# Performance work log

Hardware: AMD Instinct MI355X
Metric: run time of the kernel (lower is better)

## Reference

```python
import jax, jax.numpy as jnp
import numpy as np

D_MODEL = 256
N_HEAD = 8
D_FF = 1024
B = 8
N_PER = 4096
NQ = B * N_PER
L = 16
NEG_INF = -1e9
EPS = 1e-5


def layer_norm(x, g, b):
    mu = jnp.mean(x, axis=-1, keepdims=True)
    var = jnp.mean(jnp.square(x - mu), axis=-1, keepdims=True)
    return (x - mu) * jax.lax.rsqrt(var + EPS) * g + b


def setup_inputs() -> dict:
    key = jax.random.key(0)
    ks = jax.random.split(key, 20)
    s = 1.0 / np.sqrt(D_MODEL)
    sf = 1.0 / np.sqrt(D_FF)
    inp = {
        "src": jax.random.normal(ks[0], (NQ, D_MODEL), jnp.float32),
        "pos": jax.random.normal(ks[1], (NQ, D_MODEL), jnp.float32),
        # per-batch-relative neighbor indices in [-1, N_PER); -1 == invalid/padded
        "index_pair": jax.random.randint(ks[2], (NQ, L), 0, N_PER + 1, jnp.int32) - 1,
        "query_batch_cnt": jnp.full((B,), N_PER, jnp.int32),
        "key_batch_cnt": jnp.full((B,), N_PER, jnp.int32),
        "index_pair_batch": (jnp.arange(NQ, dtype=jnp.int32) // N_PER).astype(jnp.int32),
        "Wq": jax.random.normal(ks[3], (D_MODEL, D_MODEL), jnp.float32) * s,
        "bq": jnp.zeros((D_MODEL,), jnp.float32),
        "Wk": jax.random.normal(ks[4], (D_MODEL, D_MODEL), jnp.float32) * s,
        "bk": jnp.zeros((D_MODEL,), jnp.float32),
        "Wv": jax.random.normal(ks[5], (D_MODEL, D_MODEL), jnp.float32) * s,
        "bv": jnp.zeros((D_MODEL,), jnp.float32),
        "Wo": jax.random.normal(ks[6], (D_MODEL, D_MODEL), jnp.float32) * s,
        "bo": jnp.zeros((D_MODEL,), jnp.float32),
        "W1": jax.random.normal(ks[7], (D_MODEL, D_FF), jnp.float32) * s,
        "b1": jnp.zeros((D_FF,), jnp.float32),
        "W2": jax.random.normal(ks[8], (D_FF, D_MODEL), jnp.float32) * sf,
        "b2": jnp.zeros((D_MODEL,), jnp.float32),
        "g1": jnp.ones((D_MODEL,), jnp.float32),
        "be1": jnp.zeros((D_MODEL,), jnp.float32),
        "g2": jnp.ones((D_MODEL,), jnp.float32),
        "be2": jnp.zeros((D_MODEL,), jnp.float32),
    }
    return inp


def local_attn(q, k, v, index_pair, key_batch_cnt, index_pair_batch,
               Wq, bq, Wk, bk, Wv, bv, Wo, bo):
    H, hd = N_HEAD, D_MODEL // N_HEAD
    scale = 1.0 / np.sqrt(hd)
    qh = (q @ Wq + bq).reshape(NQ, H, hd) * scale        # [Nq,H,hd]
    kh = (k @ Wk + bk).reshape(NQ, H, hd)                # [Nk,H,hd] (Nk==Nq)
    vh = (v @ Wv + bv).reshape(NQ, H, hd)
    # start offset of each batch's keys in the stacked key tensor
    offs = jnp.cumsum(key_batch_cnt) - key_batch_cnt      # [B]
    valid = index_pair >= 0                               # [Nq,L]
    gidx = jnp.where(valid, index_pair + offs[index_pair_batch][:, None], 0)
    k_g = kh[gidx]                                        # [Nq,L,H,hd]
    v_g = vh[gidx]                                        # [Nq,L,H,hd]
    logits = jnp.einsum('nhd,nlhd->nhl', qh, k_g)         # [Nq,H,L]
    logits = jnp.where(valid[:, None, :], logits, NEG_INF)
    attn = jax.nn.softmax(logits, axis=-1)
    out = jnp.einsum('nhl,nlhd->nhd', attn, v_g).reshape(NQ, D_MODEL)
    return out @ Wo + bo


def reference(src, pos, index_pair, query_batch_cnt, key_batch_cnt, index_pair_batch,
              Wq, bq, Wk, bk, Wv, bv, Wo, bo, W1, b1, W2, b2, g1, be1, g2, be2):
    # forward_post (normalize_before=False), dropout==0 (eval)
    qk = src + pos
    src2 = local_attn(qk, qk, src, index_pair, key_batch_cnt, index_pair_batch,
                      Wq, bq, Wk, bk, Wv, bv, Wo, bo)
    x = layer_norm(src + src2, g1, be1)
    ff = jax.nn.relu(x @ W1 + b1) @ W2 + b2
    return layer_norm(x + ff, g2, be2)
```

## Files before the change

kernel.cpp:

```cpp
#include <hip/hip_runtime.h>
#include <hip/hip_bf16.h>
#include <cstdint>
#include <cstddef>

#define NQ_ 32768
#define DM_ 256
#define DFF_ 1024
#define LNB_ 16
#define NB_ 8

typedef __attribute__((ext_vector_type(4))) float f32x4;
typedef __attribute__((ext_vector_type(8))) short s16x8;

__device__ __forceinline__ float bf2f(ushort u) {
    union { unsigned int i; float f; } c; c.i = ((unsigned int)u) << 16; return c.f;
}
__device__ __forceinline__ ushort f2bf(float f) {
    union { float f; unsigned int i; } c; c.f = f;
    unsigned int x = c.i;
    return (ushort)((x + 0x7fffu + ((x >> 16) & 1u)) >> 16);
}


__global__ __launch_bounds__(256) void prep_qk(const float* __restrict__ src, const float* __restrict__ pos,
                                               ushort* __restrict__ qkb, ushort* __restrict__ srcb) {
    int i = (blockIdx.x * 256 + threadIdx.x) * 4;
    float4 s = *(const float4*)(src + i);
    float4 p = *(const float4*)(pos + i);
    ushort4 a, b;
    a.x = f2bf(s.x + p.x); a.y = f2bf(s.y + p.y); a.z = f2bf(s.z + p.z); a.w = f2bf(s.w + p.w);
    b.x = f2bf(s.x);       b.y = f2bf(s.y);       b.z = f2bf(s.z);       b.w = f2bf(s.w);
    *(ushort4*)(qkb + i) = a;
    *(ushort4*)(srcb + i) = b;
}

__global__ __launch_bounds__(256) void prep_weights(const float* __restrict__ Wq, const float* __restrict__ Wk,
                                                    const float* __restrict__ Wv, const float* __restrict__ Wo,
                                                    const float* __restrict__ W1, const float* __restrict__ W2,
                                                    const int* __restrict__ kbc,
                                                    const float* __restrict__ bq, const float* __restrict__ bk,
                                                    ushort* __restrict__ WqT, ushort* __restrict__ WkT,
                                                    ushort* __restrict__ WvT, ushort* __restrict__ WoT,
                                                    ushort* __restrict__ W1T, ushort* __restrict__ W2T,
                                                    int* __restrict__ offs, float* __restrict__ bias2) {
    const int b = blockIdx.x;
    const int t = threadIdx.x;
    if (b == 3072) {
        if (t == 0) { int a = 0; for (int i = 0; i < NB_; ++i) { offs[i] = a; a += kbc[i]; } }
        bias2[t] = bq[t];
        bias2[256 + t] = bk[t];
        return;
    }
    const float* W; ushort* Wt; int base, ks, ns;
    if (b < 1024) {
        const int sec = b >> 8;
        W  = sec == 0 ? Wq  : sec == 1 ? Wk  : sec == 2 ? Wv  : Wo;
        Wt = sec == 0 ? WqT : sec == 1 ? WkT : sec == 2 ? WvT : WoT;
        base = (b & 255) * 256; ks = 8; ns = 8;
    } else if (b < 2048) {
        W = W1; Wt = W1T; base = (b - 1024) * 256; ks = 8; ns = 10;
    } else {
        W = W2; Wt = W2T; base = (b - 2048) * 256; ks = 10; ns = 8;
    }
    const int i = base + t;
    const int n = i >> ks, k = i & ((1 << ks) - 1);
    Wt[i] = f2bf(W[(k << ns) + n]);
}


__device__ __forceinline__ void gld_lds16(const ushort* g, ushort* l) {
    __builtin_amdgcn_global_load_lds((const __attribute__((address_space(1))) void*)g,
                                     (__attribute__((address_space(3))) void*)l, 16, 0, 0);
}

template <bool RELU>
__global__ __launch_bounds__(256) void gemm_kernel(const ushort* __restrict__ A, const ushort* __restrict__ Bt,
                                                   const float* __restrict__ bias, ushort* __restrict__ C,
                                                   int M, int N, int K, float alpha) {
    __shared__ __align__(16) ushort As[2 * 128 * 32];
    __shared__ __align__(16) ushort Bs[2 * 128 * 32];
    const int tid = threadIdx.x;
    const int lane = tid & 63;
    const int wave = tid >> 6;
    const int wr = wave >> 1, wc = wave & 1;

    const int b = (int)(blockIdx.y * gridDim.x + blockIdx.x);
    const int idx = b >> 3;
    const int xt = (b & 7) * 32 + (idx & 31);
    const int yt = idx >> 5;
    const long m0 = (long)xt * 128;
    const long n0 = (long)yt * 128;

    f32x4 acc[4][4] = {};

    const int c0 = tid, c1 = tid + 256;
    const int ar0 = c0 >> 2, ac0 = c0 & 3;
    const int ar1 = c1 >> 2, ac1 = c1 & 3;
    const int as0 = (ac0 ^ ((ar0 >> 1) & 3)) * 8;
    const int as1 = (ac1 ^ ((ar1 >> 1) & 3)) * 8;
    const int la = lane & 15;
    const int sx = ((lane >> 4) ^ ((la >> 1) & 3)) * 8;

    const ushort* Ar0 = A + (m0 + ar0) * K + as0;
    const ushort* Ar1 = A + (m0 + ar1) * K + as1;
    const ushort* Br0 = Bt + (n0 + ar0) * K + as0;
    const ushort* Br1 = Bt + (n0 + ar1) * K + as1;

    const int nt = K >> 5;
    int boff = 0;
    gld_lds16(Ar0, As + c0 * 8);
    gld_lds16(Ar1, As + c1 * 8);
    gld_lds16(Br0, Bs + c0 * 8);
    gld_lds16(Br1, Bs + c1 * 8);

    for (int t = 0; t < nt; ++t) {
        if (t + 1 < nt) {
            const int kt = (t + 1) << 5;
            const int nb = boff ^ 4096;
            gld_lds16(Ar0 + kt, As + nb + c0 * 8);
            gld_lds16(Ar1 + kt, As + nb + c1 * 8);
            gld_lds16(Br0 + kt, Bs + nb + c0 * 8);
            gld_lds16(Br1 + kt, Bs + nb + c1 * 8);
            asm volatile("s_waitcnt vmcnt(4)" ::: "memory");
        } else {
            asm volatile("s_waitcnt vmcnt(0)" ::: "memory");
        }
        __builtin_amdgcn_s_barrier();
        s16x8 af[4], bfr[4];
#pragma unroll
        for (int m = 0; m < 4; ++m)
            af[m] = *(const s16x8*)(As + boff + (wr * 64 + m * 16 + la) * 32 + sx);
#pragma unroll
        for (int n = 0; n < 4; ++n)
            bfr[n] = *(const s16x8*)(Bs + boff + (wc * 64 + n * 16 + la) * 32 + sx);
        asm volatile("s_waitcnt lgkmcnt(0)" ::: "memory");
        __builtin_amdgcn_s_barrier();
#pragma unroll
        for (int m = 0; m < 4; ++m)
#pragma unroll
            for (int n = 0; n < 4; ++n)
                acc[m][n] = __builtin_amdgcn_mfma_f32_16x16x32_bf16(af[m], bfr[n], acc[m][n], 0, 0, 0);
        boff ^= 4096;
    }

#pragma unroll
    for (int n = 0; n < 4; ++n) {
        const long col = n0 + wc * 64 + n * 16 + la;
        const float bv = bias[col];
#pragma unroll
        for (int m = 0; m < 4; ++m) {
#pragma unroll
            for (int j = 0; j < 4; ++j) {
                const long row = m0 + wr * 64 + m * 16 + (lane >> 4) * 4 + j;
                float r = (acc[m][n][j] + bv) * alpha;
                if (RELU) r = fmaxf(r, 0.f);
                C[row * N + col] = f2bf(r);
            }
        }
    }
}


template <bool F32OUT>
__global__ __launch_bounds__(256) void gemm_ln_kernel(const ushort* __restrict__ A, const ushort* __restrict__ Bt,
                                                      const float* __restrict__ bias,
                                                      const ushort* __restrict__ resid,
                                                      const float* __restrict__ g, const float* __restrict__ be,
                                                      void* __restrict__ outv, int K) {
    __shared__ __align__(16) ushort As[2 * 64 * 32];
    __shared__ __align__(16) ushort Bs[2 * 256 * 32];
    __shared__ float red_s[4][64];
    __shared__ float red_q[4][64];
    const int tid = threadIdx.x;
    const int lane = tid & 63;
    const int wave = tid >> 6;
    const long m0 = (long)blockIdx.x * 64;

    const int ca = tid;
    const ushort* Arow = A + (m0 + (ca >> 2)) * K + ((ca & 3) ^ ((ca >> 3) & 3)) * 8;
    const ushort* Brow[4];
#pragma unroll
    for (int i = 0; i < 4; ++i) {
        const int cb = tid + 256 * i;
        Brow[i] = Bt + (long)(cb >> 2) * K + ((cb & 3) ^ ((cb >> 3) & 3)) * 8;
    }
    const int la = lane & 15;
    const int sx = ((lane >> 4) ^ ((la >> 1) & 3)) * 8;

    f32x4 acc[4][4] = {};
    const int nt = K >> 5;
    int buf = 0;
    gld_lds16(Arow, As + ca * 8);
#pragma unroll
    for (int i = 0; i < 4; ++i)
        gld_lds16(Brow[i], Bs + (tid + 256 * i) * 8);

    for (int t = 0; t < nt; ++t) {
        const int bA = buf * 2048, bB = buf * 8192;
        if (t + 1 < nt) {
            const int kt = (t + 1) << 5;
            const int nA = (buf ^ 1) * 2048, nB = (buf ^ 1) * 8192;
            gld_lds16(Arow + kt, As + nA + ca * 8);
#pragma unroll
            for (int i = 0; i < 4; ++i)
                gld_lds16(Brow[i] + kt, Bs + nB + (tid + 256 * i) * 8);
            asm volatile("s_waitcnt vmcnt(5)" ::: "memory");
        } else {
            asm volatile("s_waitcnt vmcnt(0)" ::: "memory");
        }
        __builtin_amdgcn_s_barrier();
        s16x8 af[4], bfr[4];
#pragma unroll
        for (int m = 0; m < 4; ++m)
            af[m] = *(const s16x8*)(As + bA + (m * 16 + la) * 32 + sx);
#pragma unroll
        for (int n = 0; n < 4; ++n)
            bfr[n] = *(const s16x8*)(Bs + bB + (wave * 64 + n * 16 + la) * 32 + sx);
        asm volatile("s_waitcnt lgkmcnt(0)" ::: "memory");
        __builtin_amdgcn_s_barrier();
#pragma unroll
        for (int m = 0; m < 4; ++m)
#pragma unroll
            for (int n = 0; n < 4; ++n)
                acc[m][n] = __builtin_amdgcn_mfma_f32_16x16x32_bf16(af[m], bfr[n], acc[m][n], 0, 0, 0);
        buf ^= 1;
    }

    const int rg4 = (lane >> 4) * 4;
    float bv[4];
#pragma unroll
    for (int n = 0; n < 4; ++n) bv[n] = bias[wave * 64 + n * 16 + la];

#pragma unroll
    for (int m = 0; m < 4; ++m) {
#pragma unroll
        for (int j = 0; j < 4; ++j) {
            const int lr = m * 16 + rg4 + j;
            float s = 0.f, q = 0.f;
#pragma unroll
            for (int n = 0; n < 4; ++n) {
                const int col = wave * 64 + n * 16 + la;
                float v = acc[m][n][j] + bv[n] + bf2f(resid[(m0 + lr) * DM_ + col]);
                acc[m][n][j] = v;
                s += v; q += v * v;
            }
#pragma unroll
            for (int mk = 1; mk < 16; mk <<= 1) { s += __shfl_xor(s, mk); q += __shfl_xor(q, mk); }
            if (la == 0) { red_s[wave][lr] = s; red_q[wave][lr] = q; }
        }
    }
    __syncthreads();

    float gv[4], bev[4];
#pragma unroll
    for (int n = 0; n < 4; ++n) {
        const int col = wave * 64 + n * 16 + la;
        gv[n] = g[col]; bev[n] = be[col];
    }
#pragma unroll
    for (int m = 0; m < 4; ++m) {
#pragma unroll
        for (int j = 0; j < 4; ++j) {
            const int lr = m * 16 + rg4 + j;
            const float s = red_s[0][lr] + red_s[1][lr] + red_s[2][lr] + red_s[3][lr];
            const float q = red_q[0][lr] + red_q[1][lr] + red_q[2][lr] + red_q[3][lr];
            const float mu = s * (1.f / 256.f);
            const float rsig = rsqrtf(q * (1.f / 256.f) - mu * mu + 1e-5f);
#pragma unroll
            for (int n = 0; n < 4; ++n) {
                const int col = wave * 64 + n * 16 + la;
                const float r = (acc[m][n][j] - mu) * rsig * gv[n] + bev[n];
                if (F32OUT) ((float*)outv)[(m0 + lr) * DM_ + col] = r;
                else        ((ushort*)outv)[(m0 + lr) * DM_ + col] = f2bf(r);
            }
        }
    }
}


__global__ __launch_bounds__(256, 4) void attn_kernel(const ushort* __restrict__ QKb,
                                                      const ushort* __restrict__ Vb, const int* __restrict__ ipair,
                                                      const int* __restrict__ ipb, const int* __restrict__ offs,
                                                      ushort* __restrict__ Ob) {
    const int blk = (blockIdx.x & 7) * (NQ_ / 8 / 8) + (blockIdx.x >> 3);
    const int lane = threadIdx.x & 63;
    const int n = blk * 8 + (threadIdx.x >> 6) * 2 + (lane >> 5);
    const size_t hoff = (size_t)(lane & 31) * 8;

    float q[8];
    {
        s16x8 v = *(const s16x8*)(QKb + (size_t)n * 512 + hoff);
#pragma unroll
        for (int e = 0; e < 8; ++e) q[e] = bf2f((ushort)v[e]);
    }
    const int off = offs[ipb[n]];
    int gi[LNB_];
    float lg[LNB_];
#pragma unroll
    for (int j = 0; j < LNB_; ++j) {
        const int ip = ipair[n * LNB_ + j];
        const int g = ip >= 0 ? ip + off : 0;
        gi[j] = g;
        s16x8 v = *(const s16x8*)(QKb + (size_t)g * 512 + 256 + hoff);
        float p = 0.f;
#pragma unroll
        for (int e = 0; e < 8; ++e)
            p = fmaf(q[e], bf2f((ushort)v[e]), p);
        p += __shfl_xor(p, 1);
        p += __shfl_xor(p, 2);
        lg[j] = ip >= 0 ? p * 0.17677669529663688f : -1e9f;
    }
    float mx = lg[0];
#pragma unroll
    for (int j = 1; j < LNB_; ++j) mx = fmaxf(mx, lg[j]);
    float sum = 0.f, pw[LNB_];
#pragma unroll
    for (int j = 0; j < LNB_; ++j) { pw[j] = __expf(lg[j] - mx); sum += pw[j]; }
    const float inv = 1.f / sum;

    float acc[8] = {};
#pragma unroll
    for (int j = 0; j < LNB_; ++j) {
        s16x8 v = *(const s16x8*)(Vb + (size_t)gi[j] * DM_ + hoff);
        const float w = pw[j] * inv;
#pragma unroll
        for (int e = 0; e < 8; ++e)
            acc[e] = fmaf(w, bf2f((ushort)v[e]), acc[e]);
    }
    s16x8 o;
#pragma unroll
    for (int e = 0; e < 8; ++e) o[e] = (short)f2bf(acc[e]);
    *(s16x8*)(Ob + (size_t)n * DM_ + hoff) = o;
}


extern "C" void kernel_launch(void* const* d_in, const int* in_sizes, int n_in,
                              void* d_out, int out_size, void* d_ws, size_t ws_size,
                              hipStream_t stream) {
    const float* src = (const float*)d_in[0];
    const float* pos = (const float*)d_in[1];
    const int* ipair = (const int*)d_in[2];
    const int* kbc   = (const int*)d_in[4];
    const int* ipb   = (const int*)d_in[5];
    const float* Wq = (const float*)d_in[6];  const float* bq = (const float*)d_in[7];
    const float* Wk = (const float*)d_in[8];  const float* bk = (const float*)d_in[9];
    const float* Wv = (const float*)d_in[10]; const float* bv = (const float*)d_in[11];
    const float* Wo = (const float*)d_in[12]; const float* bo = (const float*)d_in[13];
    const float* W1 = (const float*)d_in[14]; const float* b1 = (const float*)d_in[15];
    const float* W2 = (const float*)d_in[16]; const float* b2 = (const float*)d_in[17];
    const float* g1 = (const float*)d_in[18]; const float* be1 = (const float*)d_in[19];
    const float* g2 = (const float*)d_in[20]; const float* be2 = (const float*)d_in[21];

    char* ws = (char*)d_ws;
    const size_t SB = (size_t)NQ_ * DM_ * 2;
    ushort* qkb  = (ushort*)(ws);
    ushort* srcb = (ushort*)(ws + SB);
    ushort* QKb  = (ushort*)(ws + 2 * SB);
    ushort* Vb   = (ushort*)(ws + 4 * SB);
    ushort* fb   = (ushort*)(ws + 5 * SB);
    ushort* hb   = (ushort*)(ws);
    ushort* attno = qkb;
    ushort* xb    = Vb;
    char* wb = ws + 6 * SB;
    ushort* WqT = (ushort*)(wb);
    ushort* WkT = (ushort*)(wb + 131072);
    ushort* WvT = (ushort*)(wb + 262144);
    ushort* WoT = (ushort*)(wb + 393216);
    ushort* W1T = (ushort*)(wb + 524288);
    ushort* W2T = (ushort*)(wb + 1048576);
    int* offs   = (int*)(wb + 1572864);
    float* bias2 = (float*)(wb + 1572864 + 64);

    prep_weights<<<3073, 256, 0, stream>>>(Wq, Wk, Wv, Wo, W1, W2, kbc, bq, bk,
                                           WqT, WkT, WvT, WoT, W1T, W2T, offs, bias2);
    prep_qk<<<NQ_ * DM_ / 4 / 256, 256, 0, stream>>>(src, pos, qkb, srcb);

    dim3 gqk(NQ_ / 128, 512 / 128);
    dim3 g256(NQ_ / 128, DM_ / 128);
    dim3 gff1(NQ_ / 128, DFF_ / 128);
    gemm_kernel<false><<<gqk, 256, 0, stream>>>(qkb, WqT, bias2, QKb, NQ_, 512, DM_, 1.f);
    gemm_kernel<false><<<g256, 256, 0, stream>>>(srcb, WvT, bv, Vb, NQ_, DM_, DM_, 1.f);
    attn_kernel<<<NQ_ / 8, 256, 0, stream>>>(QKb, Vb, ipair, ipb, offs, attno);
    gemm_ln_kernel<false><<<NQ_ / 64, 256, 0, stream>>>(attno, WoT, bo, srcb, g1, be1, (void*)xb, DM_);
    gemm_kernel<true><<<gff1, 256, 0, stream>>>(xb, W1T, b1, hb, NQ_, DFF_, DM_, 1.f);
    gemm_ln_kernel<true><<<NQ_ / 64, 256, 0, stream>>>(hb, W2T, b2, xb, g2, be2, d_out, DFF_);
}
```

Before: 179.3 us.

## Enlarge GEMM+LayerNorm tile to 128 rows with 8 waves in 2x4 grid

The fused GEMM+LayerNorm kernel now processes 128 rows per block with 512 threads arranged as 2 row-waves by 4 column-waves. Each block still loads the full 256-column weight tile, so weight traffic per output row is halved. The LayerNorm reduction scratch now reuses the A-tile shared memory instead of separate arrays, which keeps LDS usage bounded. The trade-off is half as many blocks (256 instead of 512), which may reduce occupancy across CUs.

```diff
diff --git a/kernel.cpp b/kernel.cpp
--- a/kernel.cpp
+++ b/kernel.cpp
@@ -162,49 +162,45 @@
 
 
 template <bool F32OUT>
-__global__ __launch_bounds__(256) void gemm_ln_kernel(const ushort* __restrict__ A, const ushort* __restrict__ Bt,
-                                                      const float* __restrict__ bias,
-                                                      const ushort* __restrict__ resid,
-                                                      const float* __restrict__ g, const float* __restrict__ be,
-                                                      void* __restrict__ outv, int K) {
-    __shared__ __align__(16) ushort As[2 * 64 * 32];
+__global__ __launch_bounds__(512, 4) void gemm_ln_kernel(const ushort* __restrict__ A, const ushort* __restrict__ Bt,
+                                                         const float* __restrict__ bias,
+                                                         const ushort* __restrict__ resid,
+                                                         const float* __restrict__ g, const float* __restrict__ be,
+                                                         void* __restrict__ outv, int K) {
+    __shared__ __align__(16) ushort As[2 * 128 * 32];
     __shared__ __align__(16) ushort Bs[2 * 256 * 32];
-    __shared__ float red_s[4][64];
-    __shared__ float red_q[4][64];
     const int tid = threadIdx.x;
     const int lane = tid & 63;
     const int wave = tid >> 6;
-    const long m0 = (long)blockIdx.x * 64;
-
-    const int ca = tid;
-    const ushort* Arow = A + (m0 + (ca >> 2)) * K + ((ca & 3) ^ ((ca >> 3) & 3)) * 8;
-    const ushort* Brow[4];
-#pragma unroll
-    for (int i = 0; i < 4; ++i) {
-        const int cb = tid + 256 * i;
-        Brow[i] = Bt + (long)(cb >> 2) * K + ((cb & 3) ^ ((cb >> 3) & 3)) * 8;
-    }
+    const int wr = wave >> 2;
+    const int wc = wave & 3;
+    const long m0 = (long)blockIdx.x * 128;
+
+    const int rel8 = ((tid & 3) ^ ((tid >> 3) & 3)) * 8;
+    const int arow = tid >> 2;
+    const ushort* Asrc  = A + (m0 + arow) * K + rel8;
+    const ushort* Bsrc0 = Bt + (long)arow * K + rel8;
+    const ushort* Bsrc1 = Bt + (long)(arow + 128) * K + rel8;
+
     const int la = lane & 15;
     const int sx = ((lane >> 4) ^ ((la >> 1) & 3)) * 8;
 
     f32x4 acc[4][4] = {};
     const int nt = K >> 5;
     int buf = 0;
-    gld_lds16(Arow, As + ca * 8);
-#pragma unroll
-    for (int i = 0; i < 4; ++i)
-        gld_lds16(Brow[i], Bs + (tid + 256 * i) * 8);
+    gld_lds16(Asrc, As + tid * 8);
+    gld_lds16(Bsrc0, Bs + tid * 8);
+    gld_lds16(Bsrc1, Bs + (tid + 512) * 8);
 
     for (int t = 0; t < nt; ++t) {
-        const int bA = buf * 2048, bB = buf * 8192;
+        const int bA = buf * 4096, bB = buf * 8192;
         if (t + 1 < nt) {
             const int kt = (t + 1) << 5;
-            const int nA = (buf ^ 1) * 2048, nB = (buf ^ 1) * 8192;
-            gld_lds16(Arow + kt, As + nA + ca * 8);
-#pragma unroll
-            for (int i = 0; i < 4; ++i)
-                gld_lds16(Brow[i] + kt, Bs + nB + (tid + 256 * i) * 8);
-            asm volatile("s_waitcnt vmcnt(5)" ::: "memory");
+            const int nA = (buf ^ 1) * 4096, nB = (buf ^ 1) * 8192;
+            gld_lds16(Asrc + kt, As + nA + tid * 8);
+            gld_lds16(Bsrc0 + kt, Bs + nB + tid * 8);
+            gld_lds16(Bsrc1 + kt, Bs + nB + (tid + 512) * 8);
+            asm volatile("s_waitcnt vmcnt(3)" ::: "memory");
         } else {
             asm volatile("s_waitcnt vmcnt(0)" ::: "memory");
         }
@@ -212,10 +208,10 @@
         s16x8 af[4], bfr[4];
 #pragma unroll
         for (int m = 0; m < 4; ++m)
-            af[m] = *(const s16x8*)(As + bA + (m * 16 + la) * 32 + sx);
+            af[m] = *(const s16x8*)(As + bA + (wr * 64 + m * 16 + la) * 32 + sx);
 #pragma unroll
         for (int n = 0; n < 4; ++n)
-            bfr[n] = *(const s16x8*)(Bs + bB + (wave * 64 + n * 16 + la) * 32 + sx);
+            bfr[n] = *(const s16x8*)(Bs + bB + (wc * 64 + n * 16 + la) * 32 + sx);
         asm volatile("s_waitcnt lgkmcnt(0)" ::: "memory");
         __builtin_amdgcn_s_barrier();
 #pragma unroll
@@ -226,27 +222,29 @@
         buf ^= 1;
     }
 
+    float* red_s = (float*)As;
+    float* red_q = (float*)As + 512;
     const int rg4 = (lane >> 4) * 4;
     float bv[4];
 #pragma unroll
-    for (int n = 0; n < 4; ++n) bv[n] = bias[wave * 64 + n * 16 + la];
+    for (int n = 0; n < 4; ++n) bv[n] = bias[wc * 64 + n * 16 + la];
 
 #pragma unroll
     for (int m = 0; m < 4; ++m) {
 #pragma unroll
         for (int j = 0; j < 4; ++j) {
-            const int lr = m * 16 + rg4 + j;
+            const int grow = wr * 64 + m * 16 + rg4 + j;
             float s = 0.f, q = 0.f;
 #pragma unroll
             for (int n = 0; n < 4; ++n) {
-                const int col = wave * 64 + n * 16 + la;
-                float v = acc[m][n][j] + bv[n] + bf2f(resid[(m0 + lr) * DM_ + col]);
+                const int col = wc * 64 + n * 16 + la;
+                float v = acc[m][n][j] + bv[n] + bf2f(resid[(m0 + grow) * DM_ + col]);
                 acc[m][n][j] = v;
                 s += v; q += v * v;
             }
 #pragma unroll
             for (int mk = 1; mk < 16; mk <<= 1) { s += __shfl_xor(s, mk); q += __shfl_xor(q, mk); }
-            if (la == 0) { red_s[wave][lr] = s; red_q[wave][lr] = q; }
+            if (la == 0) { red_s[wc * 128 + grow] = s; red_q[wc * 128 + grow] = q; }
         }
     }
     __syncthreads();
@@ -254,24 +252,24 @@
     float gv[4], bev[4];
 #pragma unroll
     for (int n = 0; n < 4; ++n) {
-        const int col = wave * 64 + n * 16 + la;
+        const int col = wc * 64 + n * 16 + la;
         gv[n] = g[col]; bev[n] = be[col];
     }
 #pragma unroll
     for (int m = 0; m < 4; ++m) {
 #pragma unroll
         for (int j = 0; j < 4; ++j) {
-            const int lr = m * 16 + rg4 + j;
-            const float s = red_s[0][lr] + red_s[1][lr] + red_s[2][lr] + red_s[3][lr];
-            const float q = red_q[0][lr] + red_q[1][lr] + red_q[2][lr] + red_q[3][lr];
+            const int grow = wr * 64 + m * 16 + rg4 + j;
+            const float s = red_s[grow] + red_s[128 + grow] + red_s[256 + grow] + red_s[384 + grow];
+            const float q = red_q[grow] + red_q[128 + grow] + red_q[256 + grow] + red_q[384 + grow];
             const float mu = s * (1.f / 256.f);
             const float rsig = rsqrtf(q * (1.f / 256.f) - mu * mu + 1e-5f);
 #pragma unroll
             for (int n = 0; n < 4; ++n) {
-                const int col = wave * 64 + n * 16 + la;
+                const int col = wc * 64 + n * 16 + la;
                 const float r = (acc[m][n][j] - mu) * rsig * gv[n] + bev[n];
-                if (F32OUT) ((float*)outv)[(m0 + lr) * DM_ + col] = r;
-                else        ((ushort*)outv)[(m0 + lr) * DM_ + col] = f2bf(r);
+                if (F32OUT) ((float*)outv)[(m0 + grow) * DM_ + col] = r;
+                else        ((ushort*)outv)[(m0 + grow) * DM_ + col] = f2bf(r);
             }
         }
     }
@@ -357,7 +355,6 @@
     ushort* srcb = (ushort*)(ws + SB);
     ushort* QKb  = (ushort*)(ws + 2 * SB);
     ushort* Vb   = (ushort*)(ws + 4 * SB);
-    ushort* fb   = (ushort*)(ws + 5 * SB);
     ushort* hb   = (ushort*)(ws);
     ushort* attno = qkb;
     ushort* xb    = Vb;
@@ -381,7 +378,7 @@
     gemm_kernel<false><<<gqk, 256, 0, stream>>>(qkb, WqT, bias2, QKb, NQ_, 512, DM_, 1.f);
     gemm_kernel<false><<<g256, 256, 0, stream>>>(srcb, WvT, bv, Vb, NQ_, DM_, DM_, 1.f);
     attn_kernel<<<NQ_ / 8, 256, 0, stream>>>(QKb, Vb, ipair, ipb, offs, attno);
-    gemm_ln_kernel<false><<<NQ_ / 64, 256, 0, stream>>>(attno, WoT, bo, srcb, g1, be1, (void*)xb, DM_);
+    gemm_ln_kernel<false><<<NQ_ / 128, 512, 0, stream>>>(attno, WoT, bo, srcb, g1, be1, (void*)xb, DM_);
     gemm_kernel<true><<<gff1, 256, 0, stream>>>(xb, W1T, b1, hb, NQ_, DFF_, DM_, 1.f);
-    gemm_ln_kernel<true><<<NQ_ / 64, 256, 0, stream>>>(hb, W2T, b2, xb, g2, be2, d_out, DFF_);
-}
+    gemm_ln_kernel<true><<<NQ_ / 128, 512, 0, stream>>>(hb, W2T, b2, xb, g2, be2, d_out, DFF_);
+}
```

New measurement: 183.8 us. 2.6% more time.
